# Performance work log

Hardware: AMD Instinct MI355X
Metric: run time of the kernel (lower is better)

Reference implementation:

```python
import jax, jax.numpy as jnp
import numpy as np

N_CELLS = 200_000
N_FACES = 400_000
N_POINTS = 200_000
E_CF = 800_000
E_FP = 800_000
E_PP = 1_200_000
IN_C, IN_F, HID, OUT = 8, 8, 64, 128


def setup_inputs() -> dict:
    key = jax.random.key(0)
    ks = jax.random.split(key, 18)
    return {
        "x_centers": jax.random.normal(ks[0], (N_CELLS, IN_C), jnp.float32),
        "x_face": jax.random.normal(ks[1], (N_FACES, IN_F), jnp.float32),
        "W_cf": jax.random.normal(ks[2], (IN_C, HID), jnp.float32) * 0.1,
        "b_cf": jax.random.normal(ks[3], (HID,), jnp.float32) * 0.1,
        "W_fp": jax.random.normal(ks[4], (HID + IN_F, OUT), jnp.float32) * 0.1,
        "b_fp": jax.random.normal(ks[5], (OUT,), jnp.float32) * 0.1,
        "W_pp": jax.random.normal(ks[6], (OUT, OUT), jnp.float32) * 0.1,
        "W_pp_root": jax.random.normal(ks[7], (OUT, OUT), jnp.float32) * 0.1,
        "b_pp": jax.random.normal(ks[8], (OUT,), jnp.float32) * 0.1,
        "ea_cf": jax.random.uniform(ks[9], (E_CF,), jnp.float32),
        "ea_fp": jax.random.uniform(ks[10], (E_FP,), jnp.float32),
        "ea_pp": jax.random.uniform(ks[11], (E_PP,), jnp.float32),
        "src_cf": jax.random.randint(ks[12], (E_CF,), 0, N_CELLS, jnp.int32),
        "dst_cf": jax.random.randint(ks[13], (E_CF,), 0, N_FACES, jnp.int32),
        "src_fp": jax.random.randint(ks[14], (E_FP,), 0, N_FACES, jnp.int32),
        "dst_fp": jax.random.randint(ks[15], (E_FP,), 0, N_POINTS, jnp.int32),
        "src_pp": jax.random.randint(ks[16], (E_PP,), 0, N_POINTS, jnp.int32),
        "dst_pp": jax.random.randint(ks[17], (E_PP,), 0, N_POINTS, jnp.int32),
    }


def _graph_conv(x, W, b, src, dst, ea, n_dst):
    # transform-then-gather (small in-dim GEMM first), weight by edge_attr, scatter-sum
    h = x @ W                                   # [n_src, out]
    msg = h[src] * ea[:, None]                  # [E, out]
    return jax.ops.segment_sum(msg, dst, num_segments=n_dst) + b


def reference(x_centers, x_face, W_cf, b_cf, W_fp, b_fp, W_pp, W_pp_root, b_pp,
              ea_cf, ea_fp, ea_pp, src_cf, dst_cf, src_fp, dst_fp, src_pp, dst_pp):
    # layerCenterFace: cells -> faces
    y_face = _graph_conv(x_centers, W_cf, b_cf, src_cf, dst_cf, ea_cf, N_FACES)
    # concat learned face features with raw face features
    x = jnp.concatenate([y_face, x_face], axis=-1)          # [N_FACES, 72]
    # layerFacePoint: faces -> points
    y_pt = _graph_conv(x, W_fp, b_fp, src_fp, dst_fp, ea_fp, N_POINTS)
    # layerPointPoint: points -> points with root/self term
    msg = (y_pt @ W_pp)[src_pp] * ea_pp[:, None]            # [E_PP, 128]
    agg = jax.ops.segment_sum(msg, dst_pp, num_segments=N_POINTS)
    return y_pt @ W_pp_root + agg + b_pp                    # [N_POINTS, 128]
```

## Files before the change

kernel.cpp:

```cpp
#include <hip/hip_runtime.h>
#include <hip/hip_bf16.h>

#define N_CELLS  200000
#define N_FACES  400000
#define N_POINTS 200000
#define E_CF     800000
#define E_FP     800000
#define E_PP     1200000
#define CAP_CF   16
#define CAP_FP   24
#define CAP_PP   32
#define OVF_CAP  4096
#define LDA128   136

typedef __attribute__((ext_vector_type(8))) short bf16x8;
typedef __attribute__((ext_vector_type(8))) unsigned short u16x8;
typedef __attribute__((ext_vector_type(4))) float f32x4;

__device__ __forceinline__ float bf2f(unsigned short u) {
    union { unsigned int i; float f; } v; v.i = ((unsigned int)u) << 16; return v.f;
}
__device__ __forceinline__ unsigned short f2bf(float f) {
    __hip_bfloat16 h = __float2bfloat16(f);
    return *reinterpret_cast<unsigned short*>(&h);
}
__device__ __forceinline__ int2 ldnt2(const int2* p) {
    long long v = __builtin_nontemporal_load((const long long*)p);
    int2 r; r.x = (int)(v & 0xffffffffLL); r.y = (int)(v >> 32); return r;
}

__device__ __forceinline__ void fill_fixed(const int* __restrict__ src,
                                           const int* __restrict__ dst,
                                           const float* __restrict__ ea,
                                           int nE, int rlo, int rhi, int cap,
                                           int tid0, int stride,
                                           int* __restrict__ cnt,
                                           int2* __restrict__ pe,
                                           int* __restrict__ ovfn,
                                           int4* __restrict__ ovf) {
    for (int e = tid0; e < nE; e += stride) {
        int4 d4 = *(const int4*)(dst + e);
        int4 s4 = *(const int4*)(src + e);
        float4 w4 = *(const float4*)(ea + e);
        int dd[4] = {d4.x, d4.y, d4.z, d4.w};
        int ss[4] = {s4.x, s4.y, s4.z, s4.w};
        float ww[4] = {w4.x, w4.y, w4.z, w4.w};
#pragma unroll
        for (int i = 0; i < 4; ++i) {
            int d = dd[i];
            if (d >= rlo && d < rhi) {
                int t = atomicAdd(&cnt[d], 1);
                if (t < cap)
                    pe[(size_t)d * cap + t] = make_int2(ss[i], __float_as_int(ww[i]));
                else {
                    int g = atomicAdd(ovfn, 1);
                    if (g < OVF_CAP) ovf[g] = make_int4(d, ss[i], __float_as_int(ww[i]), 0);
                }
            }
        }
    }
}

__global__ __launch_bounds__(256) void k_fillA(const int* __restrict__ src_cf,
                                               const int* __restrict__ dst_cf,
                                               const float* __restrict__ ea_cf,
                                               int* __restrict__ cnt_cf,
                                               int2* __restrict__ pe_cf,
                                               const int* __restrict__ src_fp,
                                               const int* __restrict__ dst_fp,
                                               const float* __restrict__ ea_fp,
                                               int* __restrict__ cnt_fp,
                                               int2* __restrict__ pe_fp,
                                               int* __restrict__ ovfn,
                                               int4* __restrict__ ovf_cf,
                                               int4* __restrict__ ovf_fp,
                                               const float* __restrict__ W_cf,
                                               const float* __restrict__ b_cf,
                                               const float* __restrict__ W_fp,
                                               const float* __restrict__ b_fp,
                                               const float* __restrict__ W_rt,
                                               const float* __restrict__ W_pp,
                                               float* __restrict__ Wt,
                                               unsigned short* __restrict__ Bp_fin) {
    __shared__ float WcfS[512];
    __shared__ float bcfS[64];
    int b = blockIdx.x;
    if (b < 512) {
        int p = b & 3;
        int blk = b >> 2;
        int rlo = p * 100000, rhi = rlo + 100000;
        int tid0 = (blk * 256 + (int)threadIdx.x) * 4;
        fill_fixed(src_cf, dst_cf, ea_cf, E_CF, rlo, rhi, CAP_CF,
                   tid0, 128 * 256 * 4, cnt_cf, pe_cf, ovfn, ovf_cf);
    } else if (b < 1024) {
        int bb = b - 512;
        int p = bb & 3;
        int blk = bb >> 2;
        int rlo = p * 50000, rhi = rlo + 50000;
        int tid0 = (blk * 256 + (int)threadIdx.x) * 4;
        fill_fixed(src_fp, dst_fp, ea_fp, E_FP, rlo, rhi, CAP_FP,
                   tid0, 128 * 256 * 4, cnt_fp, pe_fp, ovfn + 1, ovf_fp);
    } else if (b < 1152) {
        int t = (b - 1024) * 256 + threadIdx.x;
        int j = t & 7, lane = (t >> 3) & 63, ct = (t >> 9) & 7, ks = t >> 12;
        int k = ks * 32 + ((lane >> 4) & 3) * 8 + j;
        int col = ct * 16 + (lane & 15);
        float v = (k < 128) ? W_rt[k * 128 + col] : W_pp[(k - 128) * 128 + col];
        Bp_fin[t] = f2bf(v);
    } else {
        for (int i = threadIdx.x; i < 512; i += 256) WcfS[i] = W_cf[i];
        if (threadIdx.x < 64) bcfS[threadIdx.x] = b_cf[threadIdx.x];
        __syncthreads();
        int t = threadIdx.x;
        int j = t & 127;
        if (t < 128) {
            float accW[8] = {};
            float accb = 0.f;
            for (int m = 0; m < 64; ++m) {
                float wf = W_fp[m * 128 + j];
#pragma unroll
                for (int k = 0; k < 8; ++k) accW[k] += WcfS[k * 64 + m] * wf;
                accb += bcfS[m] * wf;
            }
#pragma unroll
            for (int k = 0; k < 8; ++k) Wt[k * 128 + j] = accW[k];
            Wt[16 * 128 + j] = accb;
        } else {
#pragma unroll
            for (int k = 0; k < 8; ++k) Wt[(8 + k) * 128 + j] = W_fp[(64 + k) * 128 + j];
            Wt[17 * 128 + j] = b_fp[j];
        }
    }
}

__global__ __launch_bounds__(256) void k_fillB(const int* __restrict__ src_pp,
                                               const int* __restrict__ dst_pp,
                                               const float* __restrict__ ea_pp,
                                               int* __restrict__ cnt_pp,
                                               int2* __restrict__ pe_pp,
                                               int* __restrict__ ovfn,
                                               int4* __restrict__ ovf_pp,
                                               const float* __restrict__ xc,
                                               const int* __restrict__ cnt_cf,
                                               const int2* __restrict__ pe_cf,
                                               const int* __restrict__ ovfn_cf,
                                               const int4* __restrict__ ovf_cf,
                                               const float* __restrict__ x_face,
                                               float* __restrict__ aggcx) {
    int b = blockIdx.x;
    if (b < 512) {
        int p = b & 3;
        int blk = b >> 2;
        int rlo = p * 50000, rhi = rlo + 50000;
        int tid0 = (blk * 256 + (int)threadIdx.x) * 4;
        fill_fixed(src_pp, dst_pp, ea_pp, E_PP, rlo, rhi, CAP_PP,
                   tid0, 128 * 256 * 4, cnt_pp, pe_pp, ovfn + 2, ovf_pp);
        return;
    }
    int r = (b - 512) * 256 + threadIdx.x;
    if (r >= N_FACES) return;
    int n = cnt_cf[r]; if (n > CAP_CF) n = CAP_CF;
    const int2* prow = pe_cf + (size_t)r * CAP_CF;
    float a[8] = {};
    int e = 0;
    for (; e + 1 < n; e += 2) {
        int2 q0 = prow[e], q1 = prow[e + 1];
        float w0 = __int_as_float(q0.y), w1 = __int_as_float(q1.y);
        const float* p0 = xc + (size_t)q0.x * 8;
        const float* p1 = xc + (size_t)q1.x * 8;
        float4 u0 = *(const float4*)p0, u1 = *(const float4*)(p0 + 4);
        float4 v0 = *(const float4*)p1, v1 = *(const float4*)(p1 + 4);
        a[0] += w0 * u0.x + w1 * v0.x; a[1] += w0 * u0.y + w1 * v0.y;
        a[2] += w0 * u0.z + w1 * v0.z; a[3] += w0 * u0.w + w1 * v0.w;
        a[4] += w0 * u1.x + w1 * v1.x; a[5] += w0 * u1.y + w1 * v1.y;
        a[6] += w0 * u1.z + w1 * v1.z; a[7] += w0 * u1.w + w1 * v1.w;
    }
    if (e < n) {
        int2 q0 = prow[e];
        float w0 = __int_as_float(q0.y);
        const float* p0 = xc + (size_t)q0.x * 8;
        float4 u0 = *(const float4*)p0, u1 = *(const float4*)(p0 + 4);
        a[0] += w0 * u0.x; a[1] += w0 * u0.y; a[2] += w0 * u0.z; a[3] += w0 * u0.w;
        a[4] += w0 * u1.x; a[5] += w0 * u1.y; a[6] += w0 * u1.z; a[7] += w0 * u1.w;
    }
    int no = *ovfn_cf;
    if (no > 0) {
        if (no > OVF_CAP) no = OVF_CAP;
        for (int i = 0; i < no; ++i) {
            int4 o = ovf_cf[i];
            if (o.x == r) {
                float w0 = __int_as_float(o.z);
                const float* p0 = xc + (size_t)o.y * 8;
#pragma unroll
                for (int k = 0; k < 8; ++k) a[k] += w0 * p0[k];
            }
        }
    }
    float4 xf0 = *(const float4*)(x_face + (size_t)r * 8);
    float4 xf1 = *(const float4*)(x_face + (size_t)r * 8 + 4);
    float4* o4 = (float4*)(aggcx + (size_t)r * 16);
    o4[0] = make_float4(a[0], a[1], a[2], a[3]);
    o4[1] = make_float4(a[4], a[5], a[6], a[7]);
    o4[2] = xf0;
    o4[3] = xf1;
}

__global__ __launch_bounds__(256) void k_g17(const float* __restrict__ aggcx,
                                             const int* __restrict__ cnt,
                                             const int2* __restrict__ pe,
                                             const int* __restrict__ ovfn,
                                             const int4* __restrict__ ovf,
                                             const float* __restrict__ Wt,
                                             unsigned short* __restrict__ y_ptb) {
    __shared__ float WtS[18 * 128];
    for (int i = threadIdx.x; i < 18 * 128; i += 256) WtS[i] = Wt[i];
    __syncthreads();
    const int grp = threadIdx.x >> 4;
    const int l = threadIdx.x & 15;
    const int row = blockIdx.x * 16 + grp;
    int n = cnt[row]; if (n > CAP_FP) n = CAP_FP;
    const int2* prow = pe + (size_t)row * CAP_FP;
    float acc = 0.f, s = 0.f;
    int e = 0;
    for (; e + 1 < n; e += 2) {
        int2 q0 = ldnt2(prow + e);
        int2 q1 = ldnt2(prow + e + 1);
        float w0 = __int_as_float(q0.y), w1 = __int_as_float(q1.y);
        acc += w0 * aggcx[(size_t)q0.x * 16 + l] + w1 * aggcx[(size_t)q1.x * 16 + l];
        s += w0 + w1;
    }
    if (e < n) {
        int2 q0 = ldnt2(prow + e);
        float w0 = __int_as_float(q0.y);
        acc += w0 * aggcx[(size_t)q0.x * 16 + l];
        s += w0;
    }
    int no = *ovfn;
    if (no > 0) {
        if (no > OVF_CAP) no = OVF_CAP;
        for (int i = 0; i < no; ++i) {
            int4 o = ovf[i];
            if (o.x == row) {
                float w0 = __int_as_float(o.z);
                acc += w0 * aggcx[(size_t)o.y * 16 + l];
                s += w0;
            }
        }
    }
    const int jc = l * 8;
    float a2[8];
    {
        const float4* bb = (const float4*)(WtS + 17 * 128 + jc);
        const float4* ss4 = (const float4*)(WtS + 16 * 128 + jc);
        float4 b0 = bb[0], b1 = bb[1], s0 = ss4[0], s1 = ss4[1];
        a2[0] = b0.x + s * s0.x; a2[1] = b0.y + s * s0.y;
        a2[2] = b0.z + s * s0.z; a2[3] = b0.w + s * s0.w;
        a2[4] = b1.x + s * s1.x; a2[5] = b1.y + s * s1.y;
        a2[6] = b1.z + s * s1.z; a2[7] = b1.w + s * s1.w;
    }
#pragma unroll
    for (int k = 0; k < 16; ++k) {
        float av = __shfl(acc, k, 16);
        const float4* wr = (const float4*)(WtS + k * 128 + jc);
        float4 w0 = wr[0], w1 = wr[1];
        a2[0] += av * w0.x; a2[1] += av * w0.y; a2[2] += av * w0.z; a2[3] += av * w0.w;
        a2[4] += av * w1.x; a2[5] += av * w1.y; a2[6] += av * w1.z; a2[7] += av * w1.w;
    }
    u16x8 o0;
#pragma unroll
    for (int i = 0; i < 8; ++i) o0[i] = f2bf(a2[i]);
    *(u16x8*)(y_ptb + (size_t)row * 128 + jc) = o0;
}

__global__ __launch_bounds__(256) void k_gpp_fin(const unsigned short* __restrict__ feat,
                                                 const int* __restrict__ cnt,
                                                 const int2* __restrict__ pe,
                                                 const int* __restrict__ ovfn,
                                                 const int4* __restrict__ ovf,
                                                 const unsigned short* __restrict__ A1,
                                                 const unsigned short* __restrict__ Bp,
                                                 const float* __restrict__ bias,
                                                 float* __restrict__ out) {
    __shared__ __align__(16) unsigned short Asub[32 * LDA128];
    const int w = threadIdx.x >> 6;
    const int lane = threadIdx.x & 63;
    const int l = lane & 31;
    const int R0 = blockIdx.x * 32;
    for (int rr = 0; rr < 4; ++rr) {
        int row = R0 + w * 8 + rr * 2 + (lane >> 5);
        int n = cnt[row]; if (n > CAP_PP) n = CAP_PP;
        const int2* prow = pe + (size_t)row * CAP_PP;
        float a0 = 0.f, a1 = 0.f, a2 = 0.f, a3 = 0.f;
        int e = 0;
        for (; e + 3 < n; e += 4) {
            int2 q0 = ldnt2(prow + e),     q1 = ldnt2(prow + e + 1);
            int2 q2 = ldnt2(prow + e + 2), q3 = ldnt2(prow + e + 3);
            float w0 = __int_as_float(q0.y), w1 = __int_as_float(q1.y);
            float w2 = __int_as_float(q2.y), w3 = __int_as_float(q3.y);
            const unsigned short* f0 = feat + ((size_t)q0.x << 7) + l;
            const unsigned short* f1 = feat + ((size_t)q1.x << 7) + l;
            const unsigned short* f2 = feat + ((size_t)q2.x << 7) + l;
            const unsigned short* f3 = feat + ((size_t)q3.x << 7) + l;
            a0 += w0 * bf2f(f0[0])  + w1 * bf2f(f1[0])  + w2 * bf2f(f2[0])  + w3 * bf2f(f3[0]);
            a1 += w0 * bf2f(f0[32]) + w1 * bf2f(f1[32]) + w2 * bf2f(f2[32]) + w3 * bf2f(f3[32]);
            a2 += w0 * bf2f(f0[64]) + w1 * bf2f(f1[64]) + w2 * bf2f(f2[64]) + w3 * bf2f(f3[64]);
            a3 += w0 * bf2f(f0[96]) + w1 * bf2f(f1[96]) + w2 * bf2f(f2[96]) + w3 * bf2f(f3[96]);
        }
        for (; e < n; ++e) {
            int2 q0 = ldnt2(prow + e);
            float w0 = __int_as_float(q0.y);
            const unsigned short* f0 = feat + ((size_t)q0.x << 7) + l;
            a0 += w0 * bf2f(f0[0]);  a1 += w0 * bf2f(f0[32]);
            a2 += w0 * bf2f(f0[64]); a3 += w0 * bf2f(f0[96]);
        }
        int no = *ovfn;
        if (no > 0) {
            if (no > OVF_CAP) no = OVF_CAP;
            for (int i = 0; i < no; ++i) {
                int4 o = ovf[i];
                if (o.x == row) {
                    float w0 = __int_as_float(o.z);
                    const unsigned short* f0 = feat + ((size_t)o.y << 7) + l;
                    a0 += w0 * bf2f(f0[0]);  a1 += w0 * bf2f(f0[32]);
                    a2 += w0 * bf2f(f0[64]); a3 += w0 * bf2f(f0[96]);
                }
            }
        }
        int lr = row - R0;
        Asub[lr * LDA128 + l]      = f2bf(a0);
        Asub[lr * LDA128 + 32 + l] = f2bf(a1);
        Asub[lr * LDA128 + 64 + l] = f2bf(a2);
        Asub[lr * LDA128 + 96 + l] = f2bf(a3);
    }
    __syncthreads();
    const int rg = w >> 1, cg = w & 1;
    bf16x8 bfr[8][4];
#pragma unroll
    for (int ks = 0; ks < 8; ++ks)
#pragma unroll
        for (int c = 0; c < 4; ++c) {
            int ct = cg * 4 + c;
            bfr[ks][c] = *(const bf16x8*)(Bp + ((size_t)(ks * 8 + ct) * 64 + lane) * 8);
        }
    f32x4 acc[4] = {};
    const unsigned short* a1p = A1 + (size_t)(R0 + rg * 16 + (lane & 15)) * 128 + ((lane >> 4) * 8);
    const unsigned short* a2p = Asub + (rg * 16 + (lane & 15)) * LDA128 + ((lane >> 4) * 8);
#pragma unroll
    for (int ks = 0; ks < 4; ++ks) {
        bf16x8 af = *(const bf16x8*)(a1p + ks * 32);
#pragma unroll
        for (int c = 0; c < 4; ++c)
            acc[c] = __builtin_amdgcn_mfma_f32_16x16x32_bf16(af, bfr[ks][c], acc[c], 0, 0, 0);
    }
#pragma unroll
    for (int ks = 0; ks < 4; ++ks) {
        bf16x8 af = *(const bf16x8*)(a2p + ks * 32);
#pragma unroll
        for (int c = 0; c < 4; ++c)
            acc[c] = __builtin_amdgcn_mfma_f32_16x16x32_bf16(af, bfr[ks + 4][c], acc[c], 0, 0, 0);
    }
    const int row0 = R0 + rg * 16;
    const int rbase = row0 + (lane >> 4) * 4;
#pragma unroll
    for (int c = 0; c < 4; ++c) {
        int gcol = cg * 64 + c * 16 + (lane & 15);
        float bv = bias[gcol];
#pragma unroll
        for (int r = 0; r < 4; ++r)
            __builtin_nontemporal_store(acc[c][r] + bv,
                                        &out[(size_t)(rbase + r) * 128 + gcol]);
    }
}

extern "C" void kernel_launch(void* const* d_in, const int* in_sizes, int n_in,
                              void* d_out, int out_size, void* d_ws, size_t ws_size,
                              hipStream_t stream) {
    const float* x_centers = (const float*)d_in[0];
    const float* x_face    = (const float*)d_in[1];
    const float* W_cf      = (const float*)d_in[2];
    const float* b_cf      = (const float*)d_in[3];
    const float* W_fp      = (const float*)d_in[4];
    const float* b_fp      = (const float*)d_in[5];
    const float* W_pp      = (const float*)d_in[6];
    const float* W_rt      = (const float*)d_in[7];
    const float* b_pp      = (const float*)d_in[8];
    const float* ea_cf     = (const float*)d_in[9];
    const float* ea_fp     = (const float*)d_in[10];
    const float* ea_pp     = (const float*)d_in[11];
    const int* src_cf      = (const int*)d_in[12];
    const int* dst_cf      = (const int*)d_in[13];
    const int* src_fp      = (const int*)d_in[14];
    const int* dst_fp      = (const int*)d_in[15];
    const int* src_pp      = (const int*)d_in[16];
    const int* dst_pp      = (const int*)d_in[17];
    float* out = (float*)d_out;

    char* ws = (char*)d_ws;
    float* aggcx           = (float*)(ws + 0);
    unsigned short* y_ptb  = (unsigned short*)(ws + 28000000);
    float* Wt              = (float*)(ws + 80000000);
    int2* pe_fp            = (int2*)(ws + 81000000);
    int2* pe_cf            = (int2*)(ws + 120000000);
    int2* pe_pp            = (int2*)(ws + 172000000);
    int*  cnt_cf           = (int*)(ws + 280000000);
    int*  cnt_fp           = (int*)(ws + 281600000);
    int*  cnt_pp           = (int*)(ws + 282400000);
    int*  ovfn             = (int*)(ws + 283200000);
    int4* ovf_cf           = (int4*)(ws + 284000000);
    int4* ovf_fp           = (int4*)(ws + 284100000);
    int4* ovf_pp           = (int4*)(ws + 284200000);
    unsigned short* Bp_fin = (unsigned short*)(ws + 284400000);

    hipMemsetAsync(cnt_cf, 0, 3200016, stream);
    k_fillA<<<1153, 256, 0, stream>>>(src_cf, dst_cf, ea_cf, cnt_cf, pe_cf,
                                      src_fp, dst_fp, ea_fp, cnt_fp, pe_fp,
                                      ovfn, ovf_cf, ovf_fp,
                                      W_cf, b_cf, W_fp, b_fp, W_rt, W_pp,
                                      Wt, Bp_fin);
    k_fillB<<<512 + 1563, 256, 0, stream>>>(src_pp, dst_pp, ea_pp, cnt_pp, pe_pp,
                                            ovfn, ovf_pp,
                                            x_centers, cnt_cf, pe_cf, ovfn, ovf_cf,
                                            x_face, aggcx);
    k_g17<<<12500, 256, 0, stream>>>(aggcx, cnt_fp, pe_fp, ovfn + 1, ovf_fp, Wt, y_ptb);
    k_gpp_fin<<<6250, 256, 0, stream>>>(y_ptb, cnt_pp, pe_pp, ovfn + 2, ovf_pp,
                                        y_ptb, Bp_fin, b_pp, out);
}
```

Baseline: 373.6 us.

## Fold point-point weights into precomputed 36x128 matrix, aggregate 16-wide features instead

Uses linearity to push W_pp and W_pp_root through the face-point layer. Each point now keeps only a 16-float aggregate plus a scalar edge-weight sum, and the final output comes from a small precomputed 36x128 combined weight table. The point-point gather therefore reads 16 floats per edge instead of 128 bf16 values, and the MFMA GEMM and the bf16 y_pt buffer are gone. The cost is an extra 17x128x128 weight product in the setup kernel and CUDA-core FMAs in the final kernel. Precision also changes from bf16 to fp32.

```diff
diff --git a/kernel.cpp b/kernel.cpp
--- a/kernel.cpp
+++ b/kernel.cpp
@@ -11,19 +11,9 @@
 #define CAP_FP   24
 #define CAP_PP   32
 #define OVF_CAP  4096
-#define LDA128   136
-
-typedef __attribute__((ext_vector_type(8))) short bf16x8;
-typedef __attribute__((ext_vector_type(8))) unsigned short u16x8;
+
 typedef __attribute__((ext_vector_type(4))) float f32x4;
 
-__device__ __forceinline__ float bf2f(unsigned short u) {
-    union { unsigned int i; float f; } v; v.i = ((unsigned int)u) << 16; return v.f;
-}
-__device__ __forceinline__ unsigned short f2bf(float f) {
-    __hip_bfloat16 h = __float2bfloat16(f);
-    return *reinterpret_cast<unsigned short*>(&h);
-}
 __device__ __forceinline__ int2 ldnt2(const int2* p) {
     long long v = __builtin_nontemporal_load((const long long*)p);
     int2 r; r.x = (int)(v & 0xffffffffLL); r.y = (int)(v >> 32); return r;
@@ -80,10 +70,11 @@
                                                const float* __restrict__ b_fp,
                                                const float* __restrict__ W_rt,
                                                const float* __restrict__ W_pp,
-                                               float* __restrict__ Wt,
-                                               unsigned short* __restrict__ Bp_fin) {
+                                               const float* __restrict__ b_pp,
+                                               float* __restrict__ WALL) {
     __shared__ float WcfS[512];
     __shared__ float bcfS[64];
+    __shared__ float WtL[18 * 128];
     int b = blockIdx.x;
     if (b < 512) {
         int p = b & 3;
@@ -100,13 +91,6 @@
         int tid0 = (blk * 256 + (int)threadIdx.x) * 4;
         fill_fixed(src_fp, dst_fp, ea_fp, E_FP, rlo, rhi, CAP_FP,
                    tid0, 128 * 256 * 4, cnt_fp, pe_fp, ovfn + 1, ovf_fp);
-    } else if (b < 1152) {
-        int t = (b - 1024) * 256 + threadIdx.x;
-        int j = t & 7, lane = (t >> 3) & 63, ct = (t >> 9) & 7, ks = t >> 12;
-        int k = ks * 32 + ((lane >> 4) & 3) * 8 + j;
-        int col = ct * 16 + (lane & 15);
-        float v = (k < 128) ? W_rt[k * 128 + col] : W_pp[(k - 128) * 128 + col];
-        Bp_fin[t] = f2bf(v);
     } else {
         for (int i = threadIdx.x; i < 512; i += 256) WcfS[i] = W_cf[i];
         if (threadIdx.x < 64) bcfS[threadIdx.x] = b_cf[threadIdx.x];
@@ -123,12 +107,31 @@
                 accb += bcfS[m] * wf;
             }
 #pragma unroll
-            for (int k = 0; k < 8; ++k) Wt[k * 128 + j] = accW[k];
-            Wt[16 * 128 + j] = accb;
+            for (int k = 0; k < 8; ++k) WtL[k * 128 + j] = accW[k];
+            WtL[16 * 128 + j] = accb;
         } else {
 #pragma unroll
-            for (int k = 0; k < 8; ++k) Wt[(8 + k) * 128 + j] = W_fp[(64 + k) * 128 + j];
-            Wt[17 * 128 + j] = b_fp[j];
+            for (int k = 0; k < 8; ++k) WtL[(8 + k) * 128 + j] = W_fp[(64 + k) * 128 + j];
+            WtL[17 * 128 + j] = b_fp[j];
+        }
+        __syncthreads();
+        for (int i = threadIdx.x; i < 36 * 128; i += 256) {
+            int r = i >> 7, jj = i & 127;
+            float acc;
+            if (r < 17) {
+                acc = 0.f;
+                for (int k = 0; k < 128; ++k) acc += WtL[r * 128 + k] * W_rt[k * 128 + jj];
+            } else if (r < 34) {
+                acc = 0.f;
+                for (int k = 0; k < 128; ++k) acc += WtL[(r - 17) * 128 + k] * W_pp[k * 128 + jj];
+            } else if (r == 34) {
+                acc = 0.f;
+                for (int k = 0; k < 128; ++k) acc += WtL[17 * 128 + k] * W_pp[k * 128 + jj];
+            } else {
+                acc = b_pp[jj];
+                for (int k = 0; k < 128; ++k) acc += WtL[17 * 128 + k] * W_rt[k * 128 + jj];
+            }
+            WALL[i] = acc;
         }
     }
 }
@@ -205,16 +208,13 @@
     o4[3] = xf1;
 }
 
-__global__ __launch_bounds__(256) void k_g17(const float* __restrict__ aggcx,
+__global__ __launch_bounds__(256) void k_g16(const float* __restrict__ aggcx,
                                              const int* __restrict__ cnt,
                                              const int2* __restrict__ pe,
                                              const int* __restrict__ ovfn,
                                              const int4* __restrict__ ovf,
-                                             const float* __restrict__ Wt,
-                                             unsigned short* __restrict__ y_ptb) {
-    __shared__ float WtS[18 * 128];
-    for (int i = threadIdx.x; i < 18 * 128; i += 256) WtS[i] = Wt[i];
-    __syncthreads();
+                                             float* __restrict__ a16,
+                                             float* __restrict__ s_fp) {
     const int grp = threadIdx.x >> 4;
     const int l = threadIdx.x & 15;
     const int row = blockIdx.x * 16 + grp;
@@ -247,129 +247,99 @@
             }
         }
     }
+    a16[(size_t)row * 16 + l] = acc;
+    if (l == 0) s_fp[row] = s;
+}
+
+__global__ __launch_bounds__(256) void k_fin(const float* __restrict__ a16,
+                                             const float* __restrict__ s_fp,
+                                             const int* __restrict__ cnt,
+                                             const int2* __restrict__ pe,
+                                             const int* __restrict__ ovfn,
+                                             const int4* __restrict__ ovf,
+                                             const float* __restrict__ WALL,
+                                             float* __restrict__ out) {
+    __shared__ float W36[36 * 128];
+    for (int i = threadIdx.x; i < 36 * 128; i += 256) W36[i] = WALL[i];
+    __syncthreads();
+    const int grp = threadIdx.x >> 4;
+    const int l = threadIdx.x & 15;
+    const int row = blockIdx.x * 16 + grp;
+    int n = cnt[row]; if (n > CAP_PP) n = CAP_PP;
+    const int2* prow = pe + (size_t)row * CAP_PP;
+    float App = 0.f, Spp = 0.f, Tpp = 0.f;
+    int e = 0;
+    for (; e + 1 < n; e += 2) {
+        int2 q0 = ldnt2(prow + e);
+        int2 q1 = ldnt2(prow + e + 1);
+        float w0 = __int_as_float(q0.y), w1 = __int_as_float(q1.y);
+        App += w0 * a16[(size_t)q0.x * 16 + l] + w1 * a16[(size_t)q1.x * 16 + l];
+        Spp += w0 * s_fp[q0.x] + w1 * s_fp[q1.x];
+        Tpp += w0 + w1;
+    }
+    if (e < n) {
+        int2 q0 = ldnt2(prow + e);
+        float w0 = __int_as_float(q0.y);
+        App += w0 * a16[(size_t)q0.x * 16 + l];
+        Spp += w0 * s_fp[q0.x];
+        Tpp += w0;
+    }
+    int no = *ovfn;
+    if (no > 0) {
+        if (no > OVF_CAP) no = OVF_CAP;
+        for (int i = 0; i < no; ++i) {
+            int4 o = ovf[i];
+            if (o.x == row) {
+                float w0 = __int_as_float(o.z);
+                App += w0 * a16[(size_t)o.y * 16 + l];
+                Spp += w0 * s_fp[o.y];
+                Tpp += w0;
+            }
+        }
+    }
+    float aown = a16[(size_t)row * 16 + l];
+    float sown = s_fp[row];
     const int jc = l * 8;
-    float a2[8];
+    float o[8];
     {
-        const float4* bb = (const float4*)(WtS + 17 * 128 + jc);
-        const float4* ss4 = (const float4*)(WtS + 16 * 128 + jc);
-        float4 b0 = bb[0], b1 = bb[1], s0 = ss4[0], s1 = ss4[1];
-        a2[0] = b0.x + s * s0.x; a2[1] = b0.y + s * s0.y;
-        a2[2] = b0.z + s * s0.z; a2[3] = b0.w + s * s0.w;
-        a2[4] = b1.x + s * s1.x; a2[5] = b1.y + s * s1.y;
-        a2[6] = b1.z + s * s1.z; a2[7] = b1.w + s * s1.w;
-    }
-#pragma unroll
-    for (int k = 0; k < 16; ++k) {
-        float av = __shfl(acc, k, 16);
-        const float4* wr = (const float4*)(WtS + k * 128 + jc);
+        const float4* bb = (const float4*)(W36 + 35 * 128 + jc);
+        const float4* sr = (const float4*)(W36 + 16 * 128 + jc);
+        const float4* Sr = (const float4*)(W36 + 33 * 128 + jc);
+        const float4* Tr = (const float4*)(W36 + 34 * 128 + jc);
+        float4 b0 = bb[0], b1 = bb[1];
+        float4 s0 = sr[0], s1 = sr[1];
+        float4 S0 = Sr[0], S1 = Sr[1];
+        float4 T0 = Tr[0], T1 = Tr[1];
+        o[0] = b0.x + sown * s0.x + Spp * S0.x + Tpp * T0.x;
+        o[1] = b0.y + sown * s0.y + Spp * S0.y + Tpp * T0.y;
+        o[2] = b0.z + sown * s0.z + Spp * S0.z + Tpp * T0.z;
+        o[3] = b0.w + sown * s0.w + Spp * S0.w + Tpp * T0.w;
+        o[4] = b1.x + sown * s1.x + Spp * S1.x + Tpp * T1.x;
+        o[5] = b1.y + sown * s1.y + Spp * S1.y + Tpp * T1.y;
+        o[6] = b1.z + sown * s1.z + Spp * S1.z + Tpp * T1.z;
+        o[7] = b1.w + sown * s1.w + Spp * S1.w + Tpp * T1.w;
+    }
+#pragma unroll
+    for (int r = 0; r < 16; ++r) {
+        float av = __shfl(aown, r, 16);
+        const float4* wr = (const float4*)(W36 + r * 128 + jc);
         float4 w0 = wr[0], w1 = wr[1];
-        a2[0] += av * w0.x; a2[1] += av * w0.y; a2[2] += av * w0.z; a2[3] += av * w0.w;
-        a2[4] += av * w1.x; a2[5] += av * w1.y; a2[6] += av * w1.z; a2[7] += av * w1.w;
-    }
-    u16x8 o0;
-#pragma unroll
-    for (int i = 0; i < 8; ++i) o0[i] = f2bf(a2[i]);
-    *(u16x8*)(y_ptb + (size_t)row * 128 + jc) = o0;
-}
-
-__global__ __launch_bounds__(256) void k_gpp_fin(const unsigned short* __restrict__ feat,
-                                                 const int* __restrict__ cnt,
-                                                 const int2* __restrict__ pe,
-                                                 const int* __restrict__ ovfn,
-                                                 const int4* __restrict__ ovf,
-                                                 const unsigned short* __restrict__ A1,
-                                                 const unsigned short* __restrict__ Bp,
-                                                 const float* __restrict__ bias,
-                                                 float* __restrict__ out) {
-    __shared__ __align__(16) unsigned short Asub[32 * LDA128];
-    const int w = threadIdx.x >> 6;
-    const int lane = threadIdx.x & 63;
-    const int l = lane & 31;
-    const int R0 = blockIdx.x * 32;
-    for (int rr = 0; rr < 4; ++rr) {
-        int row = R0 + w * 8 + rr * 2 + (lane >> 5);
-        int n = cnt[row]; if (n > CAP_PP) n = CAP_PP;
-        const int2* prow = pe + (size_t)row * CAP_PP;
-        float a0 = 0.f, a1 = 0.f, a2 = 0.f, a3 = 0.f;
-        int e = 0;
-        for (; e + 3 < n; e += 4) {
-            int2 q0 = ldnt2(prow + e),     q1 = ldnt2(prow + e + 1);
-            int2 q2 = ldnt2(prow + e + 2), q3 = ldnt2(prow + e + 3);
-            float w0 = __int_as_float(q0.y), w1 = __int_as_float(q1.y);
-            float w2 = __int_as_float(q2.y), w3 = __int_as_float(q3.y);
-            const unsigned short* f0 = feat + ((size_t)q0.x << 7) + l;
-            const unsigned short* f1 = feat + ((size_t)q1.x << 7) + l;
-            const unsigned short* f2 = feat + ((size_t)q2.x << 7) + l;
-            const unsigned short* f3 = feat + ((size_t)q3.x << 7) + l;
-            a0 += w0 * bf2f(f0[0])  + w1 * bf2f(f1[0])  + w2 * bf2f(f2[0])  + w3 * bf2f(f3[0]);
-            a1 += w0 * bf2f(f0[32]) + w1 * bf2f(f1[32]) + w2 * bf2f(f2[32]) + w3 * bf2f(f3[32]);
-            a2 += w0 * bf2f(f0[64]) + w1 * bf2f(f1[64]) + w2 * bf2f(f2[64]) + w3 * bf2f(f3[64]);
-            a3 += w0 * bf2f(f0[96]) + w1 * bf2f(f1[96]) + w2 * bf2f(f2[96]) + w3 * bf2f(f3[96]);
-        }
-        for (; e < n; ++e) {
-            int2 q0 = ldnt2(prow + e);
-            float w0 = __int_as_float(q0.y);
-            const unsigned short* f0 = feat + ((size_t)q0.x << 7) + l;
-            a0 += w0 * bf2f(f0[0]);  a1 += w0 * bf2f(f0[32]);
-            a2 += w0 * bf2f(f0[64]); a3 += w0 * bf2f(f0[96]);
-        }
-        int no = *ovfn;
-        if (no > 0) {
-            if (no > OVF_CAP) no = OVF_CAP;
-            for (int i = 0; i < no; ++i) {
-                int4 o = ovf[i];
-                if (o.x == row) {
-                    float w0 = __int_as_float(o.z);
-                    const unsigned short* f0 = feat + ((size_t)o.y << 7) + l;
-                    a0 += w0 * bf2f(f0[0]);  a1 += w0 * bf2f(f0[32]);
-                    a2 += w0 * bf2f(f0[64]); a3 += w0 * bf2f(f0[96]);
-                }
-            }
-        }
-        int lr = row - R0;
-        Asub[lr * LDA128 + l]      = f2bf(a0);
-        Asub[lr * LDA128 + 32 + l] = f2bf(a1);
-        Asub[lr * LDA128 + 64 + l] = f2bf(a2);
-        Asub[lr * LDA128 + 96 + l] = f2bf(a3);
-    }
-    __syncthreads();
-    const int rg = w >> 1, cg = w & 1;
-    bf16x8 bfr[8][4];
-#pragma unroll
-    for (int ks = 0; ks < 8; ++ks)
-#pragma unroll
-        for (int c = 0; c < 4; ++c) {
-            int ct = cg * 4 + c;
-            bfr[ks][c] = *(const bf16x8*)(Bp + ((size_t)(ks * 8 + ct) * 64 + lane) * 8);
-        }
-    f32x4 acc[4] = {};
-    const unsigned short* a1p = A1 + (size_t)(R0 + rg * 16 + (lane & 15)) * 128 + ((lane >> 4) * 8);
-    const unsigned short* a2p = Asub + (rg * 16 + (lane & 15)) * LDA128 + ((lane >> 4) * 8);
-#pragma unroll
-    for (int ks = 0; ks < 4; ++ks) {
-        bf16x8 af = *(const bf16x8*)(a1p + ks * 32);
-#pragma unroll
-        for (int c = 0; c < 4; ++c)
-            acc[c] = __builtin_amdgcn_mfma_f32_16x16x32_bf16(af, bfr[ks][c], acc[c], 0, 0, 0);
-    }
-#pragma unroll
-    for (int ks = 0; ks < 4; ++ks) {
-        bf16x8 af = *(const bf16x8*)(a2p + ks * 32);
-#pragma unroll
-        for (int c = 0; c < 4; ++c)
-            acc[c] = __builtin_amdgcn_mfma_f32_16x16x32_bf16(af, bfr[ks + 4][c], acc[c], 0, 0, 0);
-    }
-    const int row0 = R0 + rg * 16;
-    const int rbase = row0 + (lane >> 4) * 4;
-#pragma unroll
-    for (int c = 0; c < 4; ++c) {
-        int gcol = cg * 64 + c * 16 + (lane & 15);
-        float bv = bias[gcol];
-#pragma unroll
-        for (int r = 0; r < 4; ++r)
-            __builtin_nontemporal_store(acc[c][r] + bv,
-                                        &out[(size_t)(rbase + r) * 128 + gcol]);
-    }
+        o[0] += av * w0.x; o[1] += av * w0.y; o[2] += av * w0.z; o[3] += av * w0.w;
+        o[4] += av * w1.x; o[5] += av * w1.y; o[6] += av * w1.z; o[7] += av * w1.w;
+    }
+#pragma unroll
+    for (int r = 0; r < 16; ++r) {
+        float av = __shfl(App, r, 16);
+        const float4* wr = (const float4*)(W36 + (17 + r) * 128 + jc);
+        float4 w0 = wr[0], w1 = wr[1];
+        o[0] += av * w0.x; o[1] += av * w0.y; o[2] += av * w0.z; o[3] += av * w0.w;
+        o[4] += av * w1.x; o[5] += av * w1.y; o[6] += av * w1.z; o[7] += av * w1.w;
+    }
+    float* op = out + (size_t)row * 128 + jc;
+    f32x4 v0 = {o[0], o[1], o[2], o[3]};
+    f32x4 v1 = {o[4], o[5], o[6], o[7]};
+    __builtin_nontemporal_store(v0, (f32x4*)op);
+    __builtin_nontemporal_store(v1, (f32x4*)(op + 4));
 }
 
 extern "C" void kernel_launch(void* const* d_in, const int* in_sizes, int n_in,
@@ -397,11 +367,12 @@
 
     char* ws = (char*)d_ws;
     float* aggcx           = (float*)(ws + 0);
-    unsigned short* y_ptb  = (unsigned short*)(ws + 28000000);
-    float* Wt              = (float*)(ws + 80000000);
-    int2* pe_fp            = (int2*)(ws + 81000000);
-    int2* pe_cf            = (int2*)(ws + 120000000);
-    int2* pe_pp            = (int2*)(ws + 172000000);
+    float* a16             = (float*)(ws + 28000000);
+    float* s_fp            = (float*)(ws + 42000000);
+    float* WALL            = (float*)(ws + 44000000);
+    int2* pe_fp            = (int2*)(ws + 50000000);
+    int2* pe_cf            = (int2*)(ws + 90000000);
+    int2* pe_pp            = (int2*)(ws + 145000000);
     int*  cnt_cf           = (int*)(ws + 280000000);
     int*  cnt_fp           = (int*)(ws + 281600000);
     int*  cnt_pp           = (int*)(ws + 282400000);
@@ -409,19 +380,17 @@
     int4* ovf_cf           = (int4*)(ws + 284000000);
     int4* ovf_fp           = (int4*)(ws + 284100000);
     int4* ovf_pp           = (int4*)(ws + 284200000);
-    unsigned short* Bp_fin = (unsigned short*)(ws + 284400000);
-
-    hipMemsetAsync(cnt_cf, 0, 3200016, stream);
-    k_fillA<<<1153, 256, 0, stream>>>(src_cf, dst_cf, ea_cf, cnt_cf, pe_cf,
+
+    (void)hipMemsetAsync(cnt_cf, 0, 3200016, stream);
+    k_fillA<<<1025, 256, 0, stream>>>(src_cf, dst_cf, ea_cf, cnt_cf, pe_cf,
                                       src_fp, dst_fp, ea_fp, cnt_fp, pe_fp,
                                       ovfn, ovf_cf, ovf_fp,
-                                      W_cf, b_cf, W_fp, b_fp, W_rt, W_pp,
-                                      Wt, Bp_fin);
+                                      W_cf, b_cf, W_fp, b_fp, W_rt, W_pp, b_pp,
+                                      WALL);
     k_fillB<<<512 + 1563, 256, 0, stream>>>(src_pp, dst_pp, ea_pp, cnt_pp, pe_pp,
                                             ovfn, ovf_pp,
                                             x_centers, cnt_cf, pe_cf, ovfn, ovf_cf,
                                             x_face, aggcx);
-    k_g17<<<12500, 256, 0, stream>>>(aggcx, cnt_fp, pe_fp, ovfn + 1, ovf_fp, Wt, y_ptb);
-    k_gpp_fin<<<6250, 256, 0, stream>>>(y_ptb, cnt_pp, pe_pp, ovfn + 2, ovf_pp,
-                                        y_ptb, Bp_fin, b_pp, out);
-}
+    k_g16<<<12500, 256, 0, stream>>>(aggcx, cnt_fp, pe_fp, ovfn + 1, ovf_fp, a16, s_fp);
+    k_fin<<<12500, 256, 0, stream>>>(a16, s_fp, cnt_pp, pe_pp, ovfn + 2, ovf_pp, WALL, out);
+}
```

Measured after the change: 342.0 us. 1.09x faster.
